# Kernel optimization log

Hardware: AMD Instinct MI355X
Metric: run time of the kernel (lower is better)

## Reference

```python
import jax, jax.numpy as jnp
import numpy as np

DIM = 768
NUM_HEADS = 12
HEAD_DIM = DIM // NUM_HEADS  # 64
IMG_W = 32
IMG_H = 32
B = 16
N = IMG_W * IMG_H + 1  # 1025 (CLS + grid)


def setup_inputs() -> dict:
    key = jax.random.key(0)
    k1, k2, k3, k4, k5 = jax.random.split(key, 5)
    x = jax.random.normal(k1, (B, N, DIM), dtype=jnp.float32)
    W_qkv = jax.random.normal(k2, (3 * DIM, DIM), dtype=jnp.float32) * 0.02
    W_proj = jax.random.normal(k3, (DIM, DIM), dtype=jnp.float32) * 0.02
    b_proj = jax.random.normal(k4, (DIM,), dtype=jnp.float32) * 0.02
    # learned mixed-RoPE frequencies, shape (2, num_heads * head_dim//2)
    freqs = jax.random.normal(k5, (2, NUM_HEADS * (HEAD_DIM // 2)), dtype=jnp.float32) * 0.1
    return {"x": x, "W_qkv": W_qkv, "W_proj": W_proj, "b_proj": b_proj, "freqs": freqs}


def _mixed_angles(freqs):
    # t_x = t % W, t_y = t // W over the flattened grid (init_t_xy)
    t = jnp.arange(IMG_W * IMG_H, dtype=jnp.float32)
    t_x = t % IMG_W
    t_y = jnp.floor(t / IMG_W)
    # outer products -> (N-1, H, hd/2) -> (H, N-1, hd/2); angle = fx + fy
    fx = (t_x[:, None] * freqs[0][None, :]).reshape(-1, NUM_HEADS, HEAD_DIM // 2)
    fy = (t_y[:, None] * freqs[1][None, :]).reshape(-1, NUM_HEADS, HEAD_DIM // 2)
    return (fx + fy).transpose(1, 0, 2)  # (H, N-1, hd/2)


def _apply_rope(t, cos, sin):
    # t: (B, H, N-1, hd); complex multiply on (even, odd) pairs
    pairs = t.reshape(*t.shape[:-1], HEAD_DIM // 2, 2)
    x0, x1 = pairs[..., 0], pairs[..., 1]
    o0 = x0 * cos - x1 * sin
    o1 = x0 * sin + x1 * cos
    return jnp.stack([o0, o1], axis=-1).reshape(t.shape)


def reference(x, W_qkv, W_proj, b_proj, freqs):
    Bx, Nx, C = x.shape
    scale = HEAD_DIM ** -0.5
    qkv = jnp.einsum('bnc,dc->bnd', x, W_qkv)  # Linear, no bias
    qkv = qkv.reshape(Bx, Nx, 3, NUM_HEADS, HEAD_DIM).transpose(2, 0, 3, 1, 4)
    q, k, v = qkv[0], qkv[1], qkv[2]  # (B, H, N, hd)

    ang = _mixed_angles(freqs)  # (H, N-1, hd/2)
    cos, sin = jnp.cos(ang), jnp.sin(ang)  # broadcast over batch

    # rotate all tokens except the leading CLS token
    q = jnp.concatenate([q[:, :, :1], _apply_rope(q[:, :, 1:], cos, sin)], axis=2)
    k = jnp.concatenate([k[:, :, :1], _apply_rope(k[:, :, 1:], cos, sin)], axis=2)

    attn = jax.nn.softmax(jnp.einsum('bhqd,bhkd->bhqk', q * scale, k), axis=-1)
    out = jnp.einsum('bhqk,bhkd->bhqd', attn, v)  # (B, H, N, hd)
    out = out.transpose(0, 2, 1, 3).reshape(Bx, Nx, C)
    return out @ W_proj.T + b_proj
```

## Files before the change

kernel.cpp:

```cpp
#include <hip/hip_runtime.h>
#include <math.h>

#define DIM     768
#define NH      12
#define HD      64
#define NTOK    1025
#define BATCH   16
#define MTOT    (BATCH * NTOK)
#define QKVD    (3 * DIM)

typedef short  short8  __attribute__((ext_vector_type(8)));
typedef short  short4v __attribute__((ext_vector_type(4)));
typedef float  f32x4   __attribute__((ext_vector_type(4)));

typedef const __attribute__((address_space(1))) void gvoid_t;
typedef __attribute__((address_space(3)))       void lvoid_t;
typedef __attribute__((address_space(3)))       char lchar_t;
#define GLD16(gsrc, ldst) __builtin_amdgcn_global_load_lds( \
    (gvoid_t*)(gsrc), (lvoid_t*)(ldst), 16, 0, 0)

static __device__ __forceinline__ unsigned int f2bf(float f) {
    unsigned int u = __float_as_uint(f);
    u += 0x7FFFu + ((u >> 16) & 1u);
    return u >> 16;
}

static __device__ __forceinline__ float red_sum(float x) {
    x += __shfl_xor(x, 16);
    x += __shfl_xor(x, 32);
    return x;
}

__device__ __forceinline__ void cvt8(const float* __restrict__ src,
                                     unsigned short* __restrict__ dst, int i) {
    float4 a = *(const float4*)(src + (size_t)i*8);
    float4 b = *(const float4*)(src + (size_t)i*8 + 4);
    uint4 pk;
    pk.x = f2bf(a.x) | (f2bf(a.y) << 16);
    pk.y = f2bf(a.z) | (f2bf(a.w) << 16);
    pk.z = f2bf(b.x) | (f2bf(b.y) << 16);
    pk.w = f2bf(b.z) | (f2bf(b.w) << 16);
    *(uint4*)(dst + (size_t)i*8) = pk;
}

__global__ __launch_bounds__(256) void cvt_bf16_kernel(
    const float* __restrict__ x, const float* __restrict__ Wq,
    const float* __restrict__ Wp,
    unsigned short* __restrict__ xb, unsigned short* __restrict__ Wqb,
    unsigned short* __restrict__ Wpb)
{
    const int stride = gridDim.x * blockDim.x;
    const int tid = blockIdx.x * blockDim.x + threadIdx.x;
    for (int i = tid; i < MTOT*DIM/8;  i += stride) cvt8(x,  xb,  i);
    for (int i = tid; i < QKVD*DIM/8;  i += stride) cvt8(Wq, Wqb, i);
    for (int i = tid; i < DIM*DIM/8;   i += stride) cvt8(Wp, Wpb, i);
}

__global__ __launch_bounds__(256) void rope_tab_kernel(
    const float* __restrict__ freqs, float2* __restrict__ tab)
{
    const int gid = blockIdx.x * 256 + threadIdx.x;
    const int p  = gid & 31;
    const int n1 = (gid >> 5) & 1023;
    const int h  = gid >> 15;
    const float tx = (float)(n1 & 31), ty = (float)(n1 >> 5);
    const float ang = tx * freqs[h*32 + p] + ty * freqs[384 + h*32 + p];
    float s, c;
    sincosf(ang, &s, &c);
    tab[gid] = make_float2(c, s);
}

__device__ __forceinline__ void gemm_core(
    const unsigned short* __restrict__ Wb,
    const unsigned short* __restrict__ Xb,
    int D0, int T0, int maxXrow,
    short* Ws, short* Xs, f32x4 acc[4][4], int tid)
{
    const int lane = tid & 63;
    const int wu   = __builtin_amdgcn_readfirstlane(tid >> 6);
    const int wr   = wu >> 1, wc = wu & 1;
    const int l4   = lane >> 4, l15 = lane & 15;

    const int srow = lane >> 3;
    const int schk = (lane & 7) ^ srow;
    const unsigned short* wsrc[4];
    const unsigned short* xsrc[4];
#pragma unroll
    for (int i = 0; i < 4; ++i) {
        int r = wu*32 + i*8 + srow;
        wsrc[i] = Wb + (size_t)(D0 + r) * DIM + schk*8;
        int xr = T0 + r; if (xr > maxXrow) xr = maxXrow;
        xsrc[i] = Xb + (size_t)xr * DIM + schk*8;
    }

    for (int kt = 0; kt < DIM/64; ++kt) {
        __syncthreads();
#pragma unroll
        for (int i = 0; i < 4; ++i) {
            GLD16(wsrc[i] + kt*64, &Ws[(wu*4 + i) * 512]);
            GLD16(xsrc[i] + kt*64, &Xs[(wu*4 + i) * 512]);
        }
        __syncthreads();

        short8 wf[4][2], xf[4][2];
#pragma unroll
        for (int f = 0; f < 4; ++f) {
            const int rw = wr*64 + f*16 + l15;
            const int rx = wc*64 + f*16 + l15;
#pragma unroll
            for (int kf = 0; kf < 2; ++kf) {
                wf[f][kf] = *(const short8*)&Ws[rw*64 + (((kf*4 + l4) ^ (rw & 7)) << 3)];
                xf[f][kf] = *(const short8*)&Xs[rx*64 + (((kf*4 + l4) ^ (rx & 7)) << 3)];
            }
        }
        __builtin_amdgcn_s_setprio(1);
#pragma unroll
        for (int kf = 0; kf < 2; ++kf)
#pragma unroll
            for (int fm = 0; fm < 4; ++fm)
#pragma unroll
                for (int fn = 0; fn < 4; ++fn)
                    acc[fm][fn] = __builtin_amdgcn_mfma_f32_16x16x32_bf16(
                        wf[fm][kf], xf[fn][kf], acc[fm][fn], 0, 0, 0);
        __builtin_amdgcn_s_setprio(0);
    }
}

__global__ __launch_bounds__(256) void qkv_gemm_kernel(
    const unsigned short* __restrict__ Wqb, const unsigned short* __restrict__ xb,
    const float2* __restrict__ tab,
    unsigned short* __restrict__ Qb, unsigned short* __restrict__ Kb,
    unsigned short* __restrict__ Vb)
{
    __shared__ __align__(16) short Ws[128*64];
    __shared__ __align__(16) short Xs[128*64];
    f32x4 acc[4][4] = {};
    const int tid = threadIdx.x;
    const int D0 = blockIdx.x * 128;
    const int T0 = blockIdx.y * 128;
    gemm_core(Wqb, xb, D0, T0, MTOT - 1, Ws, Xs, acc, tid);

    const int lane = tid & 63;
    const int wu = tid >> 6, wr = wu >> 1, wc = wu & 1;
    const int l4 = lane >> 4, l15 = lane & 15;
    const int which = D0 / DIM;
    unsigned short* dst = (which == 0) ? Qb : (which == 1) ? Kb : Vb;
    const float qs = (which == 0) ? 0.125f * 1.44269504089f : 1.f;

    unsigned bArr[4], nArr[4];
    bool vArr[4];
#pragma unroll
    for (int fn = 0; fn < 4; ++fn) {
        unsigned m = T0 + wc*64 + fn*16 + l15;
        vArr[fn] = m < MTOT;
        bArr[fn] = m / NTOK;
        nArr[fn] = m - bArr[fn]*NTOK;
    }
#pragma unroll
    for (int fm = 0; fm < 4; ++fm) {
        const int hcol = (D0 % DIM) + wr*64 + fm*16 + l4*4;
        const int h = hcol >> 6, dd = hcol & 63;
        const int p0 = dd >> 1;
#pragma unroll
        for (int fn = 0; fn < 4; ++fn) {
            if (!vArr[fn]) continue;
            f32x4 a = acc[fm][fn];
            const int n = nArr[fn];
            if (which < 2) {
                int n1 = n > 0 ? n - 1 : 0;
                float4 cs = *(const float4*)&tab[(size_t)(h*1024 + n1)*32 + p0];
                if (n == 0) cs = make_float4(1.f, 0.f, 1.f, 0.f);
                float e0 = a[0], od0 = a[1], e1 = a[2], od1 = a[3];
                a[0] = e0*cs.x - od0*cs.y;  a[1] = e0*cs.y + od0*cs.x;
                a[2] = e1*cs.z - od1*cs.w;  a[3] = e1*cs.w + od1*cs.z;
            }
            uint2 pk;
            pk.x = f2bf(a[0]*qs) | (f2bf(a[1]*qs) << 16);
            pk.y = f2bf(a[2]*qs) | (f2bf(a[3]*qs) << 16);
            *(uint2*)&dst[((size_t)(bArr[fn]*NH + h)*NTOK + n)*HD + dd] = pk;
        }
    }
}

__global__ __launch_bounds__(256) void attn_mfma_kernel(
    const unsigned short* __restrict__ Qb,
    const unsigned short* __restrict__ Kb,
    const unsigned short* __restrict__ Vb,
    unsigned short* __restrict__ Obf)
{
    __shared__ __align__(16) char KsR[2][8192];
    __shared__ __align__(16) char VtR[2][8192];
    __shared__ __align__(16) char PsR[4][4096];

    const int tid  = threadIdx.x;
    const int lane = tid & 63;
    const int w    = __builtin_amdgcn_readfirstlane(tid >> 6);
    const int l4   = lane >> 4, l15 = lane & 15, l7 = lane & 7;

    const int d    = blockIdx.x;
    const int xcd  = d & 7;
    const int s    = d >> 3;
    const int bh   = xcd * 24 + s / 9;
    const int q0   = (s % 9) * 128;
    const size_t base = (size_t)bh * NTOK * HD;

    short8 qf[2][2];
#pragma unroll
    for (int qg = 0; qg < 2; ++qg) {
        int qr = q0 + w*32 + qg*16 + l15;
        int qrc = qr < NTOK ? qr : NTOK - 1;
        qf[qg][0] = *(const short8*)(Qb + base + (size_t)qrc*HD + l4*8);
        qf[qg][1] = *(const short8*)(Qb + base + (size_t)qrc*HD + 32 + l4*8);
    }

    float lA = 0.f, lB = 0.f;
    f32x4 oA[4] = {}, oB[4] = {};

    const int ktokb = tid >> 3;
    const int kchk  = tid & 7;
    const int c0 = tid, c1 = tid + 256;
    const int vt0 = ((c0 >> 5) << 2) | ((c0 >> 1) & 3);
    const int vt1 = ((c1 >> 5) << 2) | ((c1 >> 1) & 3);
    const int vo0 = (((c0 >> 3) & 3) << 4) | ((c0 & 1) << 3);
    const int vo1 = (((c1 >> 3) & 3) << 4) | ((c1 & 1) << 3);
    char* Pw = &PsR[w][0];

#pragma unroll
    for (int i = 0; i < 2; ++i) {
        int tok = ktokb + i*32;
        int sc = kchk ^ (tok & 7);
        GLD16(Kb + base + (size_t)tok*HD + sc*8, &KsR[0][w*1024 + i*4096]);
    }
    GLD16(Vb + base + (size_t)vt0*HD + vo0, &VtR[0][w*1024]);
    GLD16(Vb + base + (size_t)vt1*HD + vo1, &VtR[0][4096 + w*1024]);

    for (int kt = 0; kt < 17; ++kt) {
        const int buf = kt & 1;
        __syncthreads();

        if (kt < 16) {
            const int nb = buf ^ 1;
#pragma unroll
            for (int i = 0; i < 2; ++i) {
                int tok = ktokb + i*32;
                int gk = (kt+1)*64 + tok; if (gk > NTOK-1) gk = NTOK-1;
                int sc = kchk ^ (tok & 7);
                GLD16(Kb + base + (size_t)gk*HD + sc*8, &KsR[nb][w*1024 + i*4096]);
            }
            int g0 = (kt+1)*64 + vt0; if (g0 > NTOK-1) g0 = NTOK-1;
            int g1 = (kt+1)*64 + vt1; if (g1 > NTOK-1) g1 = NTOK-1;
            GLD16(Vb + base + (size_t)g0*HD + vo0, &VtR[nb][w*1024]);
            GLD16(Vb + base + (size_t)g1*HD + vo1, &VtR[nb][4096 + w*1024]);
        }

        f32x4 sA[4] = {}, sB[4] = {};
        __builtin_amdgcn_s_setprio(1);
#pragma unroll
        for (int tg = 0; tg < 4; ++tg) {
            const int row = tg*16 + l15;
            short8 ka0 = *(const short8*)(&KsR[buf][0] + row*128 + ((l4 ^ l7) << 4));
            short8 ka1 = *(const short8*)(&KsR[buf][0] + row*128 + (((4 + l4) ^ l7) << 4));
            sA[tg] = __builtin_amdgcn_mfma_f32_16x16x32_bf16(ka0, qf[0][0], sA[tg], 0,0,0);
            sA[tg] = __builtin_amdgcn_mfma_f32_16x16x32_bf16(ka1, qf[0][1], sA[tg], 0,0,0);
            sB[tg] = __builtin_amdgcn_mfma_f32_16x16x32_bf16(ka0, qf[1][0], sB[tg], 0,0,0);
            sB[tg] = __builtin_amdgcn_mfma_f32_16x16x32_bf16(ka1, qf[1][1], sB[tg], 0,0,0);
        }
        __builtin_amdgcn_s_setprio(0);

        float pA[16], pB[16];
        if (kt == 16) {
#pragma unroll
            for (int tg = 0; tg < 4; ++tg)
#pragma unroll
                for (int r = 0; r < 4; ++r) {
                    int tok = 1024 + tg*16 + l4*4 + r;
                    float sa = (tok > 1024) ? -3e38f : sA[tg][r];
                    float sb = (tok > 1024) ? -3e38f : sB[tg][r];
                    pA[tg*4+r] = __builtin_exp2f(sa);
                    pB[tg*4+r] = __builtin_exp2f(sb);
                }
        } else {
#pragma unroll
            for (int tg = 0; tg < 4; ++tg)
#pragma unroll
                for (int r = 0; r < 4; ++r) {
                    pA[tg*4+r] = __builtin_exp2f(sA[tg][r]);
                    pB[tg*4+r] = __builtin_exp2f(sB[tg][r]);
                }
        }
        float psA = 0.f, psB = 0.f;
#pragma unroll
        for (int i = 0; i < 16; ++i) { psA += pA[i]; psB += pB[i]; }
        lA += psA;
        lB += psB;

#pragma unroll
        for (int tg = 0; tg < 4; ++tg) {
            unsigned k0a, k1a, k0b, k1b;
            asm volatile("v_cvt_pk_bf16_f32 %0, %1, %2" : "=v"(k0a) : "v"(pA[tg*4+0]), "v"(pA[tg*4+1]));
            asm volatile("v_cvt_pk_bf16_f32 %0, %1, %2" : "=v"(k1a) : "v"(pA[tg*4+2]), "v"(pA[tg*4+3]));
            asm volatile("v_cvt_pk_bf16_f32 %0, %1, %2" : "=v"(k0b) : "v"(pB[tg*4+0]), "v"(pB[tg*4+1]));
            asm volatile("v_cvt_pk_bf16_f32 %0, %1, %2" : "=v"(k1b) : "v"(pB[tg*4+2]), "v"(pB[tg*4+3]));
            const int chk = (((tg*2 + (l4 >> 1)) ^ l7) << 4) + (l4 & 1)*8;
            *(uint2*)(Pw + l15*128      + chk) = make_uint2(k0a, k1a);
            *(uint2*)(Pw + (16+l15)*128 + chk) = make_uint2(k0b, k1b);
        }
        __builtin_amdgcn_wave_barrier();

        const short8 pf00 = *(const short8*)(Pw + l15*128      + ((l4 ^ l7) << 4));
        const short8 pf01 = *(const short8*)(Pw + l15*128      + (((4+l4) ^ l7) << 4));
        const short8 pf10 = *(const short8*)(Pw + (16+l15)*128 + ((l4 ^ l7) << 4));
        const short8 pf11 = *(const short8*)(Pw + (16+l15)*128 + (((4+l4) ^ l7) << 4));

        const unsigned trb = (unsigned)(unsigned long long)
            (lchar_t*)(&VtR[buf][0] + (l4 << 10) + (l15 << 3));
        short4v r0a, r0b, r1a, r1b, r2a, r2b, r3a, r3b;

        asm volatile(
            "ds_read_b64_tr_b16 %0, %8 offset:0\n\t"
            "ds_read_b64_tr_b16 %1, %8 offset:512\n\t"
            "ds_read_b64_tr_b16 %2, %8 offset:128\n\t"
            "ds_read_b64_tr_b16 %3, %8 offset:640\n\t"
            "ds_read_b64_tr_b16 %4, %8 offset:256\n\t"
            "ds_read_b64_tr_b16 %5, %8 offset:768\n\t"
            "ds_read_b64_tr_b16 %6, %8 offset:384\n\t"
            "ds_read_b64_tr_b16 %7, %8 offset:896\n\t"
            "s_waitcnt lgkmcnt(0)"
            : "=&v"(r0a), "=&v"(r0b), "=&v"(r1a), "=&v"(r1b),
              "=&v"(r2a), "=&v"(r2b), "=&v"(r3a), "=&v"(r3b)
            : "v"(trb) : "memory");
        __builtin_amdgcn_sched_barrier(0);
        {
            short8 v0 = __builtin_shufflevector(r0a, r0b, 0,1,2,3,4,5,6,7);
            short8 v1 = __builtin_shufflevector(r1a, r1b, 0,1,2,3,4,5,6,7);
            short8 v2 = __builtin_shufflevector(r2a, r2b, 0,1,2,3,4,5,6,7);
            short8 v3 = __builtin_shufflevector(r3a, r3b, 0,1,2,3,4,5,6,7);
            __builtin_amdgcn_s_setprio(1);
            oA[0] = __builtin_amdgcn_mfma_f32_16x16x32_bf16(v0, pf00, oA[0], 0,0,0);
            oB[0] = __builtin_amdgcn_mfma_f32_16x16x32_bf16(v0, pf10, oB[0], 0,0,0);
            oA[1] = __builtin_amdgcn_mfma_f32_16x16x32_bf16(v1, pf00, oA[1], 0,0,0);
            oB[1] = __builtin_amdgcn_mfma_f32_16x16x32_bf16(v1, pf10, oB[1], 0,0,0);
            oA[2] = __builtin_amdgcn_mfma_f32_16x16x32_bf16(v2, pf00, oA[2], 0,0,0);
            oB[2] = __builtin_amdgcn_mfma_f32_16x16x32_bf16(v2, pf10, oB[2], 0,0,0);
            oA[3] = __builtin_amdgcn_mfma_f32_16x16x32_bf16(v3, pf00, oA[3], 0,0,0);
            oB[3] = __builtin_amdgcn_mfma_f32_16x16x32_bf16(v3, pf10, oB[3], 0,0,0);
            __builtin_amdgcn_s_setprio(0);
        }
        asm volatile(
            "ds_read_b64_tr_b16 %0, %8 offset:4096\n\t"
            "ds_read_b64_tr_b16 %1, %8 offset:4608\n\t"
            "ds_read_b64_tr_b16 %2, %8 offset:4224\n\t"
            "ds_read_b64_tr_b16 %3, %8 offset:4736\n\t"
            "ds_read_b64_tr_b16 %4, %8 offset:4352\n\t"
            "ds_read_b64_tr_b16 %5, %8 offset:4864\n\t"
            "ds_read_b64_tr_b16 %6, %8 offset:4480\n\t"
            "ds_read_b64_tr_b16 %7, %8 offset:4992\n\t"
            "s_waitcnt lgkmcnt(0)"
            : "=&v"(r0a), "=&v"(r0b), "=&v"(r1a), "=&v"(r1b),
              "=&v"(r2a), "=&v"(r2b), "=&v"(r3a), "=&v"(r3b)
            : "v"(trb) : "memory");
        __builtin_amdgcn_sched_barrier(0);
        {
            short8 v0 = __builtin_shufflevector(r0a, r0b, 0,1,2,3,4,5,6,7);
            short8 v1 = __builtin_shufflevector(r1a, r1b, 0,1,2,3,4,5,6,7);
            short8 v2 = __builtin_shufflevector(r2a, r2b, 0,1,2,3,4,5,6,7);
            short8 v3 = __builtin_shufflevector(r3a, r3b, 0,1,2,3,4,5,6,7);
            __builtin_amdgcn_s_setprio(1);
            oA[0] = __builtin_amdgcn_mfma_f32_16x16x32_bf16(v0, pf01, oA[0], 0,0,0);
            oB[0] = __builtin_amdgcn_mfma_f32_16x16x32_bf16(v0, pf11, oB[0], 0,0,0);
            oA[1] = __builtin_amdgcn_mfma_f32_16x16x32_bf16(v1, pf01, oA[1], 0,0,0);
            oB[1] = __builtin_amdgcn_mfma_f32_16x16x32_bf16(v1, pf11, oB[1], 0,0,0);
            oA[2] = __builtin_amdgcn_mfma_f32_16x16x32_bf16(v2, pf01, oA[2], 0,0,0);
            oB[2] = __builtin_amdgcn_mfma_f32_16x16x32_bf16(v2, pf11, oB[2], 0,0,0);
            oA[3] = __builtin_amdgcn_mfma_f32_16x16x32_bf16(v3, pf01, oA[3], 0,0,0);
            oB[3] = __builtin_amdgcn_mfma_f32_16x16x32_bf16(v3, pf11, oB[3], 0,0,0);
            __builtin_amdgcn_s_setprio(0);
        }
    }

    const float liA = 1.f / red_sum(lA);
    const float liB = 1.f / red_sum(lB);
    const int b = bh / NH, h = bh % NH;
    const int qA = q0 + w*32 + l15;
    const int qB = qA + 16;
    if (qA < NTOK) {
        unsigned short* p = Obf + ((size_t)b*NTOK + qA)*DIM + h*HD + l4*4;
#pragma unroll
        for (int dg = 0; dg < 4; ++dg) {
            uint2 pk;
            pk.x = f2bf(oA[dg][0]*liA) | (f2bf(oA[dg][1]*liA) << 16);
            pk.y = f2bf(oA[dg][2]*liA) | (f2bf(oA[dg][3]*liA) << 16);
            *(uint2*)(p + dg*16) = pk;
        }
    }
    if (qB < NTOK) {
        unsigned short* p = Obf + ((size_t)b*NTOK + qB)*DIM + h*HD + l4*4;
#pragma unroll
        for (int dg = 0; dg < 4; ++dg) {
            uint2 pk;
            pk.x = f2bf(oB[dg][0]*liB) | (f2bf(oB[dg][1]*liB) << 16);
            pk.y = f2bf(oB[dg][2]*liB) | (f2bf(oB[dg][3]*liB) << 16);
            *(uint2*)(p + dg*16) = pk;
        }
    }
}

__global__ __launch_bounds__(256) void proj_gemm_kernel(
    const unsigned short* __restrict__ Wpb, const unsigned short* __restrict__ Obf,
    const float* __restrict__ bp, float* __restrict__ out)
{
    __shared__ __align__(16) short Ws[128*64];
    __shared__ __align__(16) short Xs[128*64];
    f32x4 acc[4][4] = {};
    const int tid = threadIdx.x;
    const int D0 = blockIdx.x * 128;
    const int T0 = blockIdx.y * 128;
    gemm_core(Wpb, Obf, D0, T0, MTOT - 1, Ws, Xs, acc, tid);

    const int lane = tid & 63;
    const int wu = tid >> 6, wr = wu >> 1, wc = wu & 1;
    const int l4 = lane >> 4, l15 = lane & 15;

    unsigned mArr[4];
    bool vArr[4];
#pragma unroll
    for (int fn = 0; fn < 4; ++fn) {
        unsigned m = T0 + wc*64 + fn*16 + l15;
        mArr[fn] = m;
        vArr[fn] = m < MTOT;
    }
#pragma unroll
    for (int fm = 0; fm < 4; ++fm) {
        const int nG = D0 + wr*64 + fm*16 + l4*4;
        const float4 bias = *(const float4*)&bp[nG];
#pragma unroll
        for (int fn = 0; fn < 4; ++fn) {
            if (!vArr[fn]) continue;
            f32x4 a = acc[fm][fn];
            float4 v = make_float4(a[0]+bias.x, a[1]+bias.y, a[2]+bias.z, a[3]+bias.w);
            *(float4*)&out[(size_t)mArr[fn]*DIM + nG] = v;
        }
    }
}

extern "C" void kernel_launch(void* const* d_in, const int* in_sizes, int n_in,
                              void* d_out, int out_size, void* d_ws, size_t ws_size,
                              hipStream_t stream)
{
    const float* x     = (const float*)d_in[0];
    const float* Wqkv  = (const float*)d_in[1];
    const float* Wp    = (const float*)d_in[2];
    const float* bp    = (const float*)d_in[3];
    const float* freqs = (const float*)d_in[4];
    float* out = (float*)d_out;

    const size_t SZ = (size_t)BATCH * NH * NTOK * HD;
    unsigned short* Qb  = (unsigned short*)d_ws;
    unsigned short* Kb  = Qb + SZ;
    unsigned short* Vb  = Kb + SZ;
    unsigned short* Obf = Vb + SZ;
    unsigned short* xb  = Obf + SZ;
    unsigned short* Wqb = xb + SZ;
    unsigned short* Wpb = Wqb + (size_t)QKVD * DIM;
    float2*         tab = (float2*)(Wpb + (size_t)DIM * DIM);

    cvt_bf16_kernel<<<2048, 256, 0, stream>>>(x, Wqkv, Wp, xb, Wqb, Wpb);
    rope_tab_kernel<<<1536, 256, 0, stream>>>(freqs, tab);
    qkv_gemm_kernel<<<dim3(QKVD/128, (MTOT + 127)/128), 256, 0, stream>>>(
        Wqb, xb, tab, Qb, Kb, Vb);
    attn_mfma_kernel<<<1728, 256, 0, stream>>>(Qb, Kb, Vb, Obf);
    proj_gemm_kernel<<<dim3(DIM/128, (MTOT + 127)/128), 256, 0, stream>>>(
        Wpb, Obf, bp, out);
}
```

Before: 271.1 us.

## Remap GEMM grids for XCD locality and halve attention P staging buffer

Both GEMM kernels now use a 1D grid whose block index is remapped so that each XCD (block index mod 8) gets a contiguous run of token tiles, with all output-column tiles of a token tile processed in sequence. The aim is better L2 reuse of activation tiles within each XCD. In attention, the per-wave P staging buffer shrinks from 4KB to 2KB: P is written and consumed in two halves, each followed by its PV MFMAs, with a new swizzle. This lowers LDS footprint, which may allow higher occupancy, at the cost of an extra wave barrier per tile.

Result: no change. 268.3 us (-1.0%).

```diff
diff --git a/kernel.cpp b/kernel.cpp
--- a/kernel.cpp
+++ b/kernel.cpp
@@ -136,8 +136,14 @@
     __shared__ __align__(16) short Xs[128*64];
     f32x4 acc[4][4] = {};
     const int tid = threadIdx.x;
-    const int D0 = blockIdx.x * 128;
-    const int T0 = blockIdx.y * 128;
+
+    const int dd0 = blockIdx.x;
+    int xc, j;
+    if (dd0 >= 2304) { xc = 0; j = 288 + (dd0 - 2304); }
+    else             { xc = dd0 & 7; j = dd0 >> 3; }
+    const int D0 = (j % 18) * 128;
+    const int T0 = (xc + 8 * (j / 18)) * 128;
+
     gemm_core(Wqb, xb, D0, T0, MTOT - 1, Ws, Xs, acc, tid);
 
     const int lane = tid & 63;
@@ -190,7 +196,7 @@
 {
     __shared__ __align__(16) char KsR[2][8192];
     __shared__ __align__(16) char VtR[2][8192];
-    __shared__ __align__(16) char PsR[4][4096];
+    __shared__ __align__(16) char PsR[4][2048];
 
     const int tid  = threadIdx.x;
     const int lane = tid & 63;
@@ -224,6 +230,8 @@
     const int vo0 = (((c0 >> 3) & 3) << 4) | ((c0 & 1) << 3);
     const int vo1 = (((c1 >> 3) & 3) << 4) | ((c1 & 1) << 3);
     char* Pw = &PsR[w][0];
+    const int pwoff = ((l4 & 1) << 3);
+    const int prd   = (l4 ^ (l15 & 3)) << 4;
 
 #pragma unroll
     for (int i = 0; i < 2; ++i) {
@@ -294,86 +302,100 @@
         lA += psA;
         lB += psB;
 
-#pragma unroll
-        for (int tg = 0; tg < 4; ++tg) {
+        const unsigned trb = (unsigned)(unsigned long long)
+            (lchar_t*)(&VtR[buf][0] + (l4 << 10) + (l15 << 3));
+        short4v r0a, r0b, r1a, r1b, r2a, r2b, r3a, r3b;
+
+#pragma unroll
+        for (int tgl = 0; tgl < 2; ++tgl) {
+            const int tg = tgl;
             unsigned k0a, k1a, k0b, k1b;
             asm volatile("v_cvt_pk_bf16_f32 %0, %1, %2" : "=v"(k0a) : "v"(pA[tg*4+0]), "v"(pA[tg*4+1]));
             asm volatile("v_cvt_pk_bf16_f32 %0, %1, %2" : "=v"(k1a) : "v"(pA[tg*4+2]), "v"(pA[tg*4+3]));
             asm volatile("v_cvt_pk_bf16_f32 %0, %1, %2" : "=v"(k0b) : "v"(pB[tg*4+0]), "v"(pB[tg*4+1]));
             asm volatile("v_cvt_pk_bf16_f32 %0, %1, %2" : "=v"(k1b) : "v"(pB[tg*4+2]), "v"(pB[tg*4+3]));
-            const int chk = (((tg*2 + (l4 >> 1)) ^ l7) << 4) + (l4 & 1)*8;
-            *(uint2*)(Pw + l15*128      + chk) = make_uint2(k0a, k1a);
-            *(uint2*)(Pw + (16+l15)*128 + chk) = make_uint2(k0b, k1b);
+            const int boff = ((((tgl << 1) | (l4 >> 1)) ^ (l15 & 3)) << 4) + pwoff;
+            *(uint2*)(Pw + l15*64        + boff) = make_uint2(k0a, k1a);
+            *(uint2*)(Pw + (16 + l15)*64 + boff) = make_uint2(k0b, k1b);
         }
         __builtin_amdgcn_wave_barrier();
-
-        const short8 pf00 = *(const short8*)(Pw + l15*128      + ((l4 ^ l7) << 4));
-        const short8 pf01 = *(const short8*)(Pw + l15*128      + (((4+l4) ^ l7) << 4));
-        const short8 pf10 = *(const short8*)(Pw + (16+l15)*128 + ((l4 ^ l7) << 4));
-        const short8 pf11 = *(const short8*)(Pw + (16+l15)*128 + (((4+l4) ^ l7) << 4));
-
-        const unsigned trb = (unsigned)(unsigned long long)
-            (lchar_t*)(&VtR[buf][0] + (l4 << 10) + (l15 << 3));
-        short4v r0a, r0b, r1a, r1b, r2a, r2b, r3a, r3b;
-
-        asm volatile(
-            "ds_read_b64_tr_b16 %0, %8 offset:0\n\t"
-            "ds_read_b64_tr_b16 %1, %8 offset:512\n\t"
-            "ds_read_b64_tr_b16 %2, %8 offset:128\n\t"
-            "ds_read_b64_tr_b16 %3, %8 offset:640\n\t"
-            "ds_read_b64_tr_b16 %4, %8 offset:256\n\t"
-            "ds_read_b64_tr_b16 %5, %8 offset:768\n\t"
-            "ds_read_b64_tr_b16 %6, %8 offset:384\n\t"
-            "ds_read_b64_tr_b16 %7, %8 offset:896\n\t"
-            "s_waitcnt lgkmcnt(0)"
-            : "=&v"(r0a), "=&v"(r0b), "=&v"(r1a), "=&v"(r1b),
-              "=&v"(r2a), "=&v"(r2b), "=&v"(r3a), "=&v"(r3b)
-            : "v"(trb) : "memory");
-        __builtin_amdgcn_sched_barrier(0);
         {
+            const short8 pfA = *(const short8*)(Pw + l15*64        + prd);
+            const short8 pfB = *(const short8*)(Pw + (16 + l15)*64 + prd);
+            asm volatile(
+                "ds_read_b64_tr_b16 %0, %8 offset:0\n\t"
+                "ds_read_b64_tr_b16 %1, %8 offset:512\n\t"
+                "ds_read_b64_tr_b16 %2, %8 offset:128\n\t"
+                "ds_read_b64_tr_b16 %3, %8 offset:640\n\t"
+                "ds_read_b64_tr_b16 %4, %8 offset:256\n\t"
+                "ds_read_b64_tr_b16 %5, %8 offset:768\n\t"
+                "ds_read_b64_tr_b16 %6, %8 offset:384\n\t"
+                "ds_read_b64_tr_b16 %7, %8 offset:896\n\t"
+                "s_waitcnt lgkmcnt(0)"
+                : "=&v"(r0a), "=&v"(r0b), "=&v"(r1a), "=&v"(r1b),
+                  "=&v"(r2a), "=&v"(r2b), "=&v"(r3a), "=&v"(r3b)
+                : "v"(trb) : "memory");
+            __builtin_amdgcn_sched_barrier(0);
             short8 v0 = __builtin_shufflevector(r0a, r0b, 0,1,2,3,4,5,6,7);
             short8 v1 = __builtin_shufflevector(r1a, r1b, 0,1,2,3,4,5,6,7);
             short8 v2 = __builtin_shufflevector(r2a, r2b, 0,1,2,3,4,5,6,7);
             short8 v3 = __builtin_shufflevector(r3a, r3b, 0,1,2,3,4,5,6,7);
             __builtin_amdgcn_s_setprio(1);
-            oA[0] = __builtin_amdgcn_mfma_f32_16x16x32_bf16(v0, pf00, oA[0], 0,0,0);
-            oB[0] = __builtin_amdgcn_mfma_f32_16x16x32_bf16(v0, pf10, oB[0], 0,0,0);
-            oA[1] = __builtin_amdgcn_mfma_f32_16x16x32_bf16(v1, pf00, oA[1], 0,0,0);
-            oB[1] = __builtin_amdgcn_mfma_f32_16x16x32_bf16(v1, pf10, oB[1], 0,0,0);
-            oA[2] = __builtin_amdgcn_mfma_f32_16x16x32_bf16(v2, pf00, oA[2], 0,0,0);
-            oB[2] = __builtin_amdgcn_mfma_f32_16x16x32_bf16(v2, pf10, oB[2], 0,0,0);
-            oA[3] = __builtin_amdgcn_mfma_f32_16x16x32_bf16(v3, pf00, oA[3], 0,0,0);
-            oB[3] = __builtin_amdgcn_mfma_f32_16x16x32_bf16(v3, pf10, oB[3], 0,0,0);
+            oA[0] = __builtin_amdgcn_mfma_f32_16x16x32_bf16(v0, pfA, oA[0], 0,0,0);
+            oB[0] = __builtin_amdgcn_mfma_f32_16x16x32_bf16(v0, pfB, oB[0], 0,0,0);
+            oA[1] = __builtin_amdgcn_mfma_f32_16x16x32_bf16(v1, pfA, oA[1], 0,0,0);
+            oB[1] = __builtin_amdgcn_mfma_f32_16x16x32_bf16(v1, pfB, oB[1], 0,0,0);
+            oA[2] = __builtin_amdgcn_mfma_f32_16x16x32_bf16(v2, pfA, oA[2], 0,0,0);
+            oB[2] = __builtin_amdgcn_mfma_f32_16x16x32_bf16(v2, pfB, oB[2], 0,0,0);
+            oA[3] = __builtin_amdgcn_mfma_f32_16x16x32_bf16(v3, pfA, oA[3], 0,0,0);
+            oB[3] = __builtin_amdgcn_mfma_f32_16x16x32_bf16(v3, pfB, oB[3], 0,0,0);
             __builtin_amdgcn_s_setprio(0);
         }
-        asm volatile(
-            "ds_read_b64_tr_b16 %0, %8 offset:4096\n\t"
-            "ds_read_b64_tr_b16 %1, %8 offset:4608\n\t"
-            "ds_read_b64_tr_b16 %2, %8 offset:4224\n\t"
-            "ds_read_b64_tr_b16 %3, %8 offset:4736\n\t"
-            "ds_read_b64_tr_b16 %4, %8 offset:4352\n\t"
-            "ds_read_b64_tr_b16 %5, %8 offset:4864\n\t"
-            "ds_read_b64_tr_b16 %6, %8 offset:4480\n\t"
-            "ds_read_b64_tr_b16 %7, %8 offset:4992\n\t"
-            "s_waitcnt lgkmcnt(0)"
-            : "=&v"(r0a), "=&v"(r0b), "=&v"(r1a), "=&v"(r1b),
-              "=&v"(r2a), "=&v"(r2b), "=&v"(r3a), "=&v"(r3b)
-            : "v"(trb) : "memory");
-        __builtin_amdgcn_sched_barrier(0);
+        __builtin_amdgcn_wave_barrier();
+
+#pragma unroll
+        for (int tgl = 0; tgl < 2; ++tgl) {
+            const int tg = 2 + tgl;
+            unsigned k0a, k1a, k0b, k1b;
+            asm volatile("v_cvt_pk_bf16_f32 %0, %1, %2" : "=v"(k0a) : "v"(pA[tg*4+0]), "v"(pA[tg*4+1]));
+            asm volatile("v_cvt_pk_bf16_f32 %0, %1, %2" : "=v"(k1a) : "v"(pA[tg*4+2]), "v"(pA[tg*4+3]));
+            asm volatile("v_cvt_pk_bf16_f32 %0, %1, %2" : "=v"(k0b) : "v"(pB[tg*4+0]), "v"(pB[tg*4+1]));
+            asm volatile("v_cvt_pk_bf16_f32 %0, %1, %2" : "=v"(k1b) : "v"(pB[tg*4+2]), "v"(pB[tg*4+3]));
+            const int boff = ((((tgl << 1) | (l4 >> 1)) ^ (l15 & 3)) << 4) + pwoff;
+            *(uint2*)(Pw + l15*64        + boff) = make_uint2(k0a, k1a);
+            *(uint2*)(Pw + (16 + l15)*64 + boff) = make_uint2(k0b, k1b);
+        }
+        __builtin_amdgcn_wave_barrier();
         {
+            const short8 pfA = *(const short8*)(Pw + l15*64        + prd);
+            const short8 pfB = *(const short8*)(Pw + (16 + l15)*64 + prd);
+            asm volatile(
+                "ds_read_b64_tr_b16 %0, %8 offset:4096\n\t"
+                "ds_read_b64_tr_b16 %1, %8 offset:4608\n\t"
+                "ds_read_b64_tr_b16 %2, %8 offset:4224\n\t"
+                "ds_read_b64_tr_b16 %3, %8 offset:4736\n\t"
+                "ds_read_b64_tr_b16 %4, %8 offset:4352\n\t"
+                "ds_read_b64_tr_b16 %5, %8 offset:4864\n\t"
+                "ds_read_b64_tr_b16 %6, %8 offset:4480\n\t"
+                "ds_read_b64_tr_b16 %7, %8 offset:4992\n\t"
+                "s_waitcnt lgkmcnt(0)"
+                : "=&v"(r0a), "=&v"(r0b), "=&v"(r1a), "=&v"(r1b),
+                  "=&v"(r2a), "=&v"(r2b), "=&v"(r3a), "=&v"(r3b)
+                : "v"(trb) : "memory");
+            __builtin_amdgcn_sched_barrier(0);
             short8 v0 = __builtin_shufflevector(r0a, r0b, 0,1,2,3,4,5,6,7);
             short8 v1 = __builtin_shufflevector(r1a, r1b, 0,1,2,3,4,5,6,7);
             short8 v2 = __builtin_shufflevector(r2a, r2b, 0,1,2,3,4,5,6,7);
             short8 v3 = __builtin_shufflevector(r3a, r3b, 0,1,2,3,4,5,6,7);
             __builtin_amdgcn_s_setprio(1);
-            oA[0] = __builtin_amdgcn_mfma_f32_16x16x32_bf16(v0, pf01, oA[0], 0,0,0);
-            oB[0] = __builtin_amdgcn_mfma_f32_16x16x32_bf16(v0, pf11, oB[0], 0,0,0);
-            oA[1] = __builtin_amdgcn_mfma_f32_16x16x32_bf16(v1, pf01, oA[1], 0,0,0);
-            oB[1] = __builtin_amdgcn_mfma_f32_16x16x32_bf16(v1, pf11, oB[1], 0,0,0);
-            oA[2] = __builtin_amdgcn_mfma_f32_16x16x32_bf16(v2, pf01, oA[2], 0,0,0);
-            oB[2] = __builtin_amdgcn_mfma_f32_16x16x32_bf16(v2, pf11, oB[2], 0,0,0);
-            oA[3] = __builtin_amdgcn_mfma_f32_16x16x32_bf16(v3, pf01, oA[3], 0,0,0);
-            oB[3] = __builtin_amdgcn_mfma_f32_16x16x32_bf16(v3, pf11, oB[3], 0,0,0);
+            oA[0] = __builtin_amdgcn_mfma_f32_16x16x32_bf16(v0, pfA, oA[0], 0,0,0);
+            oB[0] = __builtin_amdgcn_mfma_f32_16x16x32_bf16(v0, pfB, oB[0], 0,0,0);
+            oA[1] = __builtin_amdgcn_mfma_f32_16x16x32_bf16(v1, pfA, oA[1], 0,0,0);
+            oB[1] = __builtin_amdgcn_mfma_f32_16x16x32_bf16(v1, pfB, oB[1], 0,0,0);
+            oA[2] = __builtin_amdgcn_mfma_f32_16x16x32_bf16(v2, pfA, oA[2], 0,0,0);
+            oB[2] = __builtin_amdgcn_mfma_f32_16x16x32_bf16(v2, pfB, oB[2], 0,0,0);
+            oA[3] = __builtin_amdgcn_mfma_f32_16x16x32_bf16(v3, pfA, oA[3], 0,0,0);
+            oB[3] = __builtin_amdgcn_mfma_f32_16x16x32_bf16(v3, pfB, oB[3], 0,0,0);
             __builtin_amdgcn_s_setprio(0);
         }
     }
@@ -413,8 +435,14 @@
     __shared__ __align__(16) short Xs[128*64];
     f32x4 acc[4][4] = {};
     const int tid = threadIdx.x;
-    const int D0 = blockIdx.x * 128;
-    const int T0 = blockIdx.y * 128;
+
+    const int dd0 = blockIdx.x;
+    int xc, j;
+    if (dd0 >= 768) { xc = 0; j = 96 + (dd0 - 768); }
+    else            { xc = dd0 & 7; j = dd0 >> 3; }
+    const int D0 = (j % 6) * 128;
+    const int T0 = (xc + 8 * (j / 6)) * 128;
+
     gemm_core(Wpb, Obf, D0, T0, MTOT - 1, Ws, Xs, acc, tid);
 
     const int lane = tid & 63;
@@ -466,9 +494,7 @@
 
     cvt_bf16_kernel<<<2048, 256, 0, stream>>>(x, Wqkv, Wp, xb, Wqb, Wpb);
     rope_tab_kernel<<<1536, 256, 0, stream>>>(freqs, tab);
-    qkv_gemm_kernel<<<dim3(QKVD/128, (MTOT + 127)/128), 256, 0, stream>>>(
-        Wqb, xb, tab, Qb, Kb, Vb);
+    qkv_gemm_kernel<<<2322, 256, 0, stream>>>(Wqb, xb, tab, Qb, Kb, Vb);
     attn_mfma_kernel<<<1728, 256, 0, stream>>>(Qb, Kb, Vb, Obf);
-    proj_gemm_kernel<<<dim3(DIM/128, (MTOT + 127)/128), 256, 0, stream>>>(
-        Wpb, Obf, bp, out);
-}
+    proj_gemm_kernel<<<774, 256, 0, stream>>>(Wpb, Obf, bp, out);
+}
```
